# Kernel tuning notes

Measured on AMD Instinct MI355X. Metric: run time of the kernel, lower is better.

Reference implementation:

```python
import jax, jax.numpy as jnp
import numpy as np

N_IN = 2048
N_OUT = 2048
RANK = 64
NUM_ITER = 4  # Newton-Schulz iterations, matches default num_iter=4


def setup_inputs() -> dict:
    key = jax.random.key(0)
    k1, k2, k3 = jax.random.split(key, 3)
    # scale U,V modestly so A = UV^T - VU^T is well-conditioned (mimics orthogonal init scale)
    scale = 1.0 / np.sqrt(N_IN)
    return {
        "input": jax.random.normal(k1, (8, 2048, N_IN), dtype=jnp.float32),
        "U": jax.random.normal(k2, (N_IN, RANK), dtype=jnp.float32) * scale,
        "V": jax.random.normal(k3, (N_IN, RANK), dtype=jnp.float32) * scale,
    }


def _orthogonal_weight(U, V):
    # A = U V^T - V U^T  (skew-symmetric, rank <= 2*rank)
    A = U @ V.T - V @ U.T              # [n, n]
    I = jnp.eye(N_IN, dtype=A.dtype)
    B = I - A
    X = I
    for _ in range(NUM_ITER):          # Newton-Schulz iteration for B^{-1}
        X = X @ (2.0 * I - B @ X)
    W_square = (I + A) @ X             # Cayley transform (I+A)(I-A)^{-1} approx
    return W_square[:N_OUT, :N_IN]


def reference(input, U, V):
    W = _orthogonal_weight(U, V)       # [out, in]
    # F.linear(input, W) = input @ W.T
    return jnp.einsum("bsi,oi->bso", input, W)
```

## Files before the change

kernel.cpp:

```cpp
#include <hip/hip_runtime.h>
#include <hip/hip_bf16.h>
#include <cstdint>
#include <cstddef>

#define NIN   2048
#define RANK  64
#define R2    128
#define NROWS 16384

typedef __bf16 bf16x8 __attribute__((ext_vector_type(8)));
typedef float  f32x4  __attribute__((ext_vector_type(4)));
typedef unsigned short u16x8 __attribute__((ext_vector_type(8)));

__device__ __forceinline__ unsigned short f2bf(float f) {
  union { float f; unsigned u; } x; x.f = f;
  return (unsigned short)((x.u + 0x7fffu + ((x.u >> 16) & 1u)) >> 16);
}

__device__ __forceinline__ void smallGemm(const float* __restrict__ A,
                                          const float* __restrict__ B,
                                          float* __restrict__ O,
                                          float a, float b, int t, int tid) {
  int i = (t >> 3) * 16 + (tid >> 4);
  int j = (t & 7) * 16 + (tid & 15);
  float acc = 0.f;
#pragma unroll 8
  for (int k = 0; k < R2; ++k) {
    float av = A[i * R2 + k]; if (k == i) av += a;
    float bv = B[k * R2 + j]; if (k == j) bv += b;
    acc += av * bv;
  }
  O[i * R2 + j] = acc;
}

__global__ __launch_bounds__(512) void k_prep(const float* __restrict__ U,
                                              const float* __restrict__ V,
                                              unsigned short* __restrict__ Mf,
                                              float* __restrict__ G) {
  __shared__ float red[512];
  int b = blockIdx.x, tid = threadIdx.x;
  if (b < 64) {
    int CI = b * 512 + tid;
    int lane = CI & 63, J = (CI >> 6) & 63, t = CI >> 12;
    int n = t * 16 + (lane & 15);
    int k0 = J * 32 + (lane >> 4) * 8;
    const float* src = (n < RANK) ? (U + n) : (V + (n - RANK));
    u16x8 h;
#pragma unroll
    for (int e = 0; e < 8; ++e) h[e] = f2bf(src[(size_t)(k0 + e) * RANK]);
    *(u16x8*)(Mf + (size_t)CI * 8) = h;
  } else {
    int tile = b - 64;
    int bi = tile >> 3, bj = tile & 7;
    int sub = tid >> 8, t256 = tid & 255;
    int ty = t256 >> 4, tx = t256 & 15;
    int i = bi * 16 + ty, j = bj * 16 + tx;
    const float* Ai = (i < RANK) ? (U + i) : (V + (i - RANK));
    const float* Aj = (j < RANK) ? (U + j) : (V + (j - RANK));
    int k0 = sub * 1024;
    float acc = 0.f;
#pragma unroll 8
    for (int k = k0; k < k0 + 1024; ++k) acc += Ai[(size_t)k * RANK] * Aj[(size_t)k * RANK];
    red[tid] = acc;
    __syncthreads();
    if (sub == 0) {
      float s = red[t256] + red[256 + t256];
      if (i < RANK) G[(i + RANK) * R2 + j] = -s;
      else          G[(i - RANK) * R2 + j] =  s;
    }
  }
}

struct SOp { const float* A; const float* B; float* O; float a, b; };
struct SOps { SOp op[3]; };
__global__ void k_small(SOps ops) {
  SOp o = ops.op[blockIdx.x >> 6];
  smallGemm(o.A, o.B, o.O, o.a, o.b, blockIdx.x & 63, threadIdx.x);
}

__global__ void k_D(const float* __restrict__ U, const float* __restrict__ V,
                    const float* __restrict__ H, const float* __restrict__ G15,
                    unsigned short* __restrict__ Df) {
  int idx = blockIdx.x * 256 + threadIdx.x;
  int i = idx >> 7, j = idx & 127;
  int jj = (j < RANK) ? (j + RANK) : (j - RANK);
  float sgn = (j < RANK) ? -1.f : 1.f;
  float acc = 0.f;
#pragma unroll 8
  for (int k = 0; k < R2; ++k) {
    float m = (k < RANK) ? U[(size_t)i * RANK + k] : V[(size_t)i * RANK + (k - RANK)];
    float t = 2.f * H[k * R2 + jj] - G15[k * R2 + jj];
    acc += m * (sgn * t);
  }
  int t_ = i >> 4, lr = i & 15;
  int J = j >> 5, lg = (j >> 3) & 3, e = j & 7;
  size_t CI = (size_t)(t_ * 4 + J) * 64 + lg * 16 + lr;
  Df[CI * 8 + e] = f2bf(acc);
}

__global__ __launch_bounds__(256) void k_T1(const float* __restrict__ input,
                                            const unsigned short* __restrict__ Mf,
                                            unsigned short* __restrict__ T1bf,
                                            const float* __restrict__ G,
                                            float* __restrict__ G2) {
  __shared__ __align__(16) unsigned char lds[73728];
  if (blockIdx.x >= 512) {
    smallGemm(G, G, G2, 0.f, 0.f, blockIdx.x - 512, threadIdx.x);
    return;
  }
  const int tid = threadIdx.x, lane = tid & 63, w = tid >> 6;
  const int lr = lane & 15, lg = lane >> 4;
  const int row0 = blockIdx.x * 32;
  unsigned char* abuf = lds + w * 8192;
  float* rbuf = (float*)lds;

  f32x4 acc[2][8] = {};
  const float* gbase = input + (size_t)row0 * NIN + w * 512;
  const int Jbase = w * 16;
  float4 s0[8], s1[8];
  bf16x8 bx[8], by[8];

#define T1_SLOAD(KT)                                                          \
  _Pragma("unroll") for (int p = 0; p < 8; ++p) {                             \
    int id = p * 64 + lane; int r = id >> 4, C = id & 15;                     \
    const float* g = gbase + (size_t)r * NIN + (KT) * 128 + C * 8;            \
    s0[p] = *(const float4*)g; s1[p] = *(const float4*)(g + 4);               \
  }
#define T1_SWRITE()                                                           \
  _Pragma("unroll") for (int p = 0; p < 8; ++p) {                             \
    int id = p * 64 + lane; int r = id >> 4, C = id & 15;                     \
    u16x8 h;                                                                  \
    h[0] = f2bf(s0[p].x); h[1] = f2bf(s0[p].y);                               \
    h[2] = f2bf(s0[p].z); h[3] = f2bf(s0[p].w);                               \
    h[4] = f2bf(s1[p].x); h[5] = f2bf(s1[p].y);                               \
    h[6] = f2bf(s1[p].z); h[7] = f2bf(s1[p].w);                               \
    *(u16x8*)(abuf + r * 256 + ((C ^ (r & 7)) << 4)) = h;                     \
  }
#define T1_BLOAD(P, S)                                                        \
  _Pragma("unroll") for (int t = 0; t < 8; ++t)                               \
    P[t] = *(const bf16x8*)(Mf + ((size_t)(t * 64 + Jbase + (S)) * 64 + lane) * 8);

  T1_SLOAD(0);
  T1_SWRITE();
  T1_BLOAD(bx, 0);
#pragma unroll
  for (int s = 0; s < 16; ++s) {
    const int kt = s >> 2, j = s & 3;
    if (j == 0 && kt < 3) { T1_SLOAD(kt + 1); }
    bf16x8 a0, a1;
    {
      int C = j * 4 + lg;
      a0 = *(const bf16x8*)(abuf + lr * 256 + ((C ^ (lr & 7)) << 4));
      a1 = *(const bf16x8*)(abuf + (16 + lr) * 256 + ((C ^ ((16 + lr) & 7)) << 4));
    }
    if (s < 15) { if (s & 1) { T1_BLOAD(bx, s + 1); } else { T1_BLOAD(by, s + 1); } }
#pragma unroll
    for (int t = 0; t < 8; ++t) {
      bf16x8 bcur = (s & 1) ? by[t] : bx[t];
      acc[0][t] = __builtin_amdgcn_mfma_f32_16x16x32_bf16(a0, bcur, acc[0][t], 0, 0, 0);
      acc[1][t] = __builtin_amdgcn_mfma_f32_16x16x32_bf16(a1, bcur, acc[1][t], 0, 0, 0);
    }
    if (j == 3 && kt < 3) { T1_SWRITE(); }
  }

  __syncthreads();
#pragma unroll
  for (int m = 0; m < 2; ++m)
#pragma unroll
    for (int t = 0; t < 8; ++t) {
      int col = t * 16 + lr, row = m * 16 + lg * 4;
      *(f32x4*)&rbuf[((size_t)w * 128 + col) * 36 + row] = acc[m][t];
    }
  __syncthreads();
  {
    int r = tid & 31, cg = tid >> 5;
    u16x8 o1, o2;
#pragma unroll
    for (int i = 0; i < 16; ++i) {
      int col = cg * 16 + i;
      float s = rbuf[(size_t)col * 36 + r]
              + rbuf[((size_t)128 + col) * 36 + r]
              + rbuf[((size_t)256 + col) * 36 + r]
              + rbuf[((size_t)384 + col) * 36 + r];
      if (i < 8) o1[i] = f2bf(s); else o2[i - 8] = f2bf(s);
    }
    unsigned short* dst = T1bf + (size_t)(row0 + r) * R2 + cg * 16;
    *(u16x8*)dst = o1;
    *(u16x8*)(dst + 8) = o2;
  }
}

__global__ __launch_bounds__(256) void k_OUT(const float* __restrict__ input,
                                             const unsigned short* __restrict__ T1bf,
                                             const unsigned short* __restrict__ Df,
                                             float* __restrict__ out) {
  __shared__ float obuf[4][32][132];
  const int tid = threadIdx.x, lane = tid & 63, w = tid >> 6;
  const int lr = lane & 15, lg = lane >> 4;
  const int row0 = blockIdx.x * 32;

  bf16x8 bq[2][4];
#pragma unroll
  for (int R = 0; R < 2; ++R)
#pragma unroll
    for (int J = 0; J < 4; ++J)
      bq[R][J] = *(const bf16x8*)(T1bf + (size_t)(row0 + R * 16 + lr) * R2 + J * 32 + lg * 8);

  bf16x8 xd[4], yd[4];
#define O_DLOAD(P, TTI)                                                       \
  _Pragma("unroll") for (int J = 0; J < 4; ++J)                               \
    P[J] = *(const bf16x8*)(Df + ((size_t)((w * 32 + (TTI)) * 4 + J) * 64 + lane) * 8);

  O_DLOAD(xd, 0);
#pragma unroll
  for (int g = 0; g < 4; ++g) {
#pragma unroll
    for (int tt = 0; tt < 8; ++tt) {
      const int tti = g * 8 + tt;
      if (tti < 31) { if (tti & 1) { O_DLOAD(xd, tti + 1); } else { O_DLOAD(yd, tti + 1); } }
#pragma unroll
      for (int R = 0; R < 2; ++R) {
        f32x4 o = {};
#pragma unroll
        for (int J = 0; J < 4; ++J) {
          bf16x8 d = (tti & 1) ? yd[J] : xd[J];
          o = __builtin_amdgcn_mfma_f32_16x16x32_bf16(d, bq[R][J], o, 0, 0, 0);
        }
        *(f32x4*)&obuf[w][R * 16 + lr][tt * 16 + lg * 4] = o;
      }
    }
#pragma unroll
    for (int c = 0; c < 16; ++c) {
      int id = c * 64 + lane;
      int r = id >> 5, cc = id & 31;
      f32x4 v = *(const f32x4*)&obuf[w][r][cc * 4];
      int grow = row0 + r, gcol = w * 512 + g * 128 + cc * 4;
      float4 inv = *(const float4*)(input + (size_t)grow * NIN + gcol);
      float4 res = { v[0] + inv.x, v[1] + inv.y, v[2] + inv.z, v[3] + inv.w };
      *(float4*)(out + (size_t)grow * NIN + gcol) = res;
    }
  }
}

extern "C" void kernel_launch(void* const* d_in, const int* in_sizes, int n_in,
                              void* d_out, int out_size, void* d_ws, size_t ws_size,
                              hipStream_t stream) {
  const float* input = (const float*)d_in[0];
  const float* U     = (const float*)d_in[1];
  const float* V     = (const float*)d_in[2];
  float* out = (float*)d_out;
  char* ws = (char*)d_ws;

  float* mats = (float*)ws;
  float* G   = mats + 0 * 16384;
  float* G2  = mats + 1 * 16384;
  float* G3  = mats + 2 * 16384;
  float* G4  = mats + 3 * 16384;
  float* G7  = mats + 4 * 16384;
  float* G8  = mats + 5 * 16384;
  float* H12 = mats + 6 * 16384;
  float* H124= mats + 7 * 16384;
  float* H   = mats + 8 * 16384;
  float* G15 = mats + 9 * 16384;
  unsigned short* Mf   = (unsigned short*)(ws + 10 * 65536);
  unsigned short* Df   = (unsigned short*)(ws + 10 * 65536 + 524288);
  unsigned short* T1bf = (unsigned short*)(ws + 10 * 65536 + 2 * 524288);

  k_prep<<<128, 512, 0, stream>>>(U, V, Mf, G);
  k_T1<<<576, 256, 0, stream>>>(input, Mf, T1bf, G, G2);

  { SOps o = {{ {G2, G2, G4, 0.f, 0.f}, {G2, G, G3, 0.f, 0.f}, {G, G2, H12, 1.f, 1.f} }};
    k_small<<<192, 256, 0, stream>>>(o); }
  { SOps o = {{ {G4, G4, G8, 0.f, 0.f}, {G3, G4, G7, 0.f, 0.f}, {H12, G4, H124, 0.f, 1.f} }};
    k_small<<<192, 256, 0, stream>>>(o); }
  { SOps o = {{ {G7, G8, G15, 0.f, 0.f}, {H124, G8, H, 0.f, 1.f}, {nullptr,nullptr,nullptr,0.f,0.f} }};
    k_small<<<128, 256, 0, stream>>>(o); }

  k_D<<<1024, 256, 0, stream>>>(U, V, H, G15, Df);
  k_OUT<<<512, 256, 0, stream>>>(input, T1bf, Df, out);
}
```

Baseline: 159.5 us.

## Fold D-matrix kernel into output kernel via reassociated low-rank product

```diff
diff --git a/kernel.cpp b/kernel.cpp
--- a/kernel.cpp
+++ b/kernel.cpp
@@ -36,6 +36,7 @@
 __global__ __launch_bounds__(512) void k_prep(const float* __restrict__ U,
                                               const float* __restrict__ V,
                                               unsigned short* __restrict__ Mf,
+                                              unsigned short* __restrict__ Mrf,
                                               float* __restrict__ G) {
   __shared__ float red[512];
   int b = blockIdx.x, tid = threadIdx.x;
@@ -49,7 +50,7 @@
 #pragma unroll
     for (int e = 0; e < 8; ++e) h[e] = f2bf(src[(size_t)(k0 + e) * RANK]);
     *(u16x8*)(Mf + (size_t)CI * 8) = h;
-  } else {
+  } else if (b < 128) {
     int tile = b - 64;
     int bi = tile >> 3, bj = tile & 7;
     int sub = tid >> 8, t256 = tid & 255;
@@ -58,16 +59,34 @@
     const float* Ai = (i < RANK) ? (U + i) : (V + (i - RANK));
     const float* Aj = (j < RANK) ? (U + j) : (V + (j - RANK));
     int k0 = sub * 1024;
-    float acc = 0.f;
-#pragma unroll 8
-    for (int k = k0; k < k0 + 1024; ++k) acc += Ai[(size_t)k * RANK] * Aj[(size_t)k * RANK];
-    red[tid] = acc;
+    float p0 = 0.f, p1 = 0.f, p2 = 0.f, p3 = 0.f;
+#pragma unroll 4
+    for (int k = k0; k < k0 + 1024; k += 4) {
+      p0 += Ai[(size_t)k * RANK]       * Aj[(size_t)k * RANK];
+      p1 += Ai[(size_t)(k + 1) * RANK] * Aj[(size_t)(k + 1) * RANK];
+      p2 += Ai[(size_t)(k + 2) * RANK] * Aj[(size_t)(k + 2) * RANK];
+      p3 += Ai[(size_t)(k + 3) * RANK] * Aj[(size_t)(k + 3) * RANK];
+    }
+    red[tid] = (p0 + p1) + (p2 + p3);
     __syncthreads();
     if (sub == 0) {
       float s = red[t256] + red[256 + t256];
       if (i < RANK) G[(i + RANK) * R2 + j] = -s;
       else          G[(i - RANK) * R2 + j] =  s;
     }
+  } else {
+    int CI = (b - 128) * 512 + tid;
+    int lane = CI & 63, rest = CI >> 6;
+    int lr = lane & 15, lg = lane >> 4;
+    int J = rest & 3, t_ = rest >> 2;
+    int i = t_ * 16 + lr, j0 = J * 32 + lg * 8;
+    const float* src = (j0 < RANK) ? (U + (size_t)i * RANK + j0)
+                                   : (V + (size_t)i * RANK + (j0 - RANK));
+    float4 f0 = *(const float4*)src, f1 = *(const float4*)(src + 4);
+    u16x8 h;
+    h[0] = f2bf(f0.x); h[1] = f2bf(f0.y); h[2] = f2bf(f0.z); h[3] = f2bf(f0.w);
+    h[4] = f2bf(f1.x); h[5] = f2bf(f1.y); h[6] = f2bf(f1.z); h[7] = f2bf(f1.w);
+    *(u16x8*)(Mrf + (size_t)CI * 8) = h;
   }
 }
 
@@ -76,26 +95,6 @@
 __global__ void k_small(SOps ops) {
   SOp o = ops.op[blockIdx.x >> 6];
   smallGemm(o.A, o.B, o.O, o.a, o.b, blockIdx.x & 63, threadIdx.x);
-}
-
-__global__ void k_D(const float* __restrict__ U, const float* __restrict__ V,
-                    const float* __restrict__ H, const float* __restrict__ G15,
-                    unsigned short* __restrict__ Df) {
-  int idx = blockIdx.x * 256 + threadIdx.x;
-  int i = idx >> 7, j = idx & 127;
-  int jj = (j < RANK) ? (j + RANK) : (j - RANK);
-  float sgn = (j < RANK) ? -1.f : 1.f;
-  float acc = 0.f;
-#pragma unroll 8
-  for (int k = 0; k < R2; ++k) {
-    float m = (k < RANK) ? U[(size_t)i * RANK + k] : V[(size_t)i * RANK + (k - RANK)];
-    float t = 2.f * H[k * R2 + jj] - G15[k * R2 + jj];
-    acc += m * (sgn * t);
-  }
-  int t_ = i >> 4, lr = i & 15;
-  int J = j >> 5, lg = (j >> 3) & 3, e = j & 7;
-  size_t CI = (size_t)(t_ * 4 + J) * 64 + lg * 16 + lr;
-  Df[CI * 8 + e] = f2bf(acc);
 }
 
 __global__ __launch_bounds__(256) void k_T1(const float* __restrict__ input,
@@ -192,24 +191,84 @@
 
 __global__ __launch_bounds__(256) void k_OUT(const float* __restrict__ input,
                                              const unsigned short* __restrict__ T1bf,
-                                             const unsigned short* __restrict__ Df,
+                                             const float* __restrict__ Hm,
+                                             const float* __restrict__ G15m,
+                                             const unsigned short* __restrict__ Mrf,
                                              float* __restrict__ out) {
-  __shared__ float obuf[4][32][132];
+  __shared__ __align__(16) unsigned char lds[75776];
+  unsigned char* cbuf = lds;
+  unsigned char* t2buf = lds + 67584;
   const int tid = threadIdx.x, lane = tid & 63, w = tid >> 6;
   const int lr = lane & 15, lg = lane >> 4;
   const int row0 = blockIdx.x * 32;
 
+#pragma unroll
+  for (int it = 0; it < 8; ++it) {
+    int id = it * 256 + tid;
+    int k = id >> 4, j8 = id & 15, j0 = j8 * 8;
+    int jj0 = (j0 < RANK) ? j0 + RANK : j0 - RANK;
+    float sgn = (j0 < RANK) ? -1.f : 1.f;
+    const float* hp = Hm + k * R2 + jj0;
+    const float* gp = G15m + k * R2 + jj0;
+    float4 h0 = *(const float4*)hp, h1 = *(const float4*)(hp + 4);
+    float4 g0 = *(const float4*)gp, g1 = *(const float4*)(gp + 4);
+    u16x8 cv;
+    cv[0] = f2bf(sgn * (2.f * h0.x - g0.x));
+    cv[1] = f2bf(sgn * (2.f * h0.y - g0.y));
+    cv[2] = f2bf(sgn * (2.f * h0.z - g0.z));
+    cv[3] = f2bf(sgn * (2.f * h0.w - g0.w));
+    cv[4] = f2bf(sgn * (2.f * h1.x - g1.x));
+    cv[5] = f2bf(sgn * (2.f * h1.y - g1.y));
+    cv[6] = f2bf(sgn * (2.f * h1.z - g1.z));
+    cv[7] = f2bf(sgn * (2.f * h1.w - g1.w));
+    *(u16x8*)(cbuf + k * 256 + ((j8 ^ (k & 7)) << 4)) = cv;
+  }
+  bf16x8 t1f[2][4];
+#pragma unroll
+  for (int R = 0; R < 2; ++R)
+#pragma unroll
+    for (int J = 0; J < 4; ++J)
+      t1f[R][J] = *(const bf16x8*)(T1bf + (size_t)(row0 + R * 16 + lr) * R2 + J * 32 + lg * 8);
+  __syncthreads();
+
+#pragma unroll
+  for (int kk = 0; kk < 2; ++kk) {
+    int kct = w * 2 + kk;
+    int kc = kct * 16 + lr;
+    f32x4 a2[2] = {};
+#pragma unroll
+    for (int jkt = 0; jkt < 4; ++jkt) {
+      bf16x8 cf = *(const bf16x8*)(cbuf + kc * 256 + (((jkt * 4 + lg) ^ (kc & 7)) << 4));
+#pragma unroll
+      for (int R = 0; R < 2; ++R)
+        a2[R] = __builtin_amdgcn_mfma_f32_16x16x32_bf16(cf, t1f[R][jkt], a2[R], 0, 0, 0);
+    }
+#pragma unroll
+    for (int R = 0; R < 2; ++R) {
+      int r = R * 16 + lr;
+      ushort4 p;
+      p.x = f2bf(a2[R][0]); p.y = f2bf(a2[R][1]);
+      p.z = f2bf(a2[R][2]); p.w = f2bf(a2[R][3]);
+      int gran = kct * 2 + (lg >> 1), off = (lg & 1) * 8;
+      *(ushort4*)(t2buf + r * 256 + ((gran ^ (r & 7)) << 4) + off) = p;
+    }
+  }
+  __syncthreads();
+
   bf16x8 bq[2][4];
 #pragma unroll
   for (int R = 0; R < 2; ++R)
 #pragma unroll
-    for (int J = 0; J < 4; ++J)
-      bq[R][J] = *(const bf16x8*)(T1bf + (size_t)(row0 + R * 16 + lr) * R2 + J * 32 + lg * 8);
-
+    for (int J = 0; J < 4; ++J) {
+      int row = R * 16 + lr;
+      bq[R][J] = *(const bf16x8*)(t2buf + row * 256 + (((J * 4 + lg) ^ (row & 7)) << 4));
+    }
+
+  float* obufw = (float*)lds + (size_t)w * 32 * 132;
   bf16x8 xd[4], yd[4];
 #define O_DLOAD(P, TTI)                                                       \
   _Pragma("unroll") for (int J = 0; J < 4; ++J)                               \
-    P[J] = *(const bf16x8*)(Df + ((size_t)((w * 32 + (TTI)) * 4 + J) * 64 + lane) * 8);
+    P[J] = *(const bf16x8*)(Mrf + ((size_t)((w * 32 + (TTI)) * 4 + J) * 64 + lane) * 8);
 
   O_DLOAD(xd, 0);
 #pragma unroll
@@ -226,14 +285,14 @@
           bf16x8 d = (tti & 1) ? yd[J] : xd[J];
           o = __builtin_amdgcn_mfma_f32_16x16x32_bf16(d, bq[R][J], o, 0, 0, 0);
         }
-        *(f32x4*)&obuf[w][R * 16 + lr][tt * 16 + lg * 4] = o;
+        *(f32x4*)&obufw[(R * 16 + lr) * 132 + tt * 16 + lg * 4] = o;
       }
     }
 #pragma unroll
     for (int c = 0; c < 16; ++c) {
       int id = c * 64 + lane;
       int r = id >> 5, cc = id & 31;
-      f32x4 v = *(const f32x4*)&obuf[w][r][cc * 4];
+      f32x4 v = *(const f32x4*)&obufw[r * 132 + cc * 4];
       int grow = row0 + r, gcol = w * 512 + g * 128 + cc * 4;
       float4 inv = *(const float4*)(input + (size_t)grow * NIN + gcol);
       float4 res = { v[0] + inv.x, v[1] + inv.y, v[2] + inv.z, v[3] + inv.w };
@@ -263,10 +322,10 @@
   float* H   = mats + 8 * 16384;
   float* G15 = mats + 9 * 16384;
   unsigned short* Mf   = (unsigned short*)(ws + 10 * 65536);
-  unsigned short* Df   = (unsigned short*)(ws + 10 * 65536 + 524288);
+  unsigned short* Mrf  = (unsigned short*)(ws + 10 * 65536 + 524288);
   unsigned short* T1bf = (unsigned short*)(ws + 10 * 65536 + 2 * 524288);
 
-  k_prep<<<128, 512, 0, stream>>>(U, V, Mf, G);
+  k_prep<<<192, 512, 0, stream>>>(U, V, Mf, Mrf, G);
   k_T1<<<576, 256, 0, stream>>>(input, Mf, T1bf, G, G2);
 
   { SOps o = {{ {G2, G2, G4, 0.f, 0.f}, {G2, G, G3, 0.f, 0.f}, {G, G2, H12, 1.f, 1.f} }};
@@ -276,6 +335,5 @@
   { SOps o = {{ {G7, G8, G15, 0.f, 0.f}, {H124, G8, H, 0.f, 1.f}, {nullptr,nullptr,nullptr,0.f,0.f} }};
     k_small<<<128, 256, 0, stream>>>(o); }
 
-  k_D<<<1024, 256, 0, stream>>>(U, V, H, G15, Df);
-  k_OUT<<<512, 256, 0, stream>>>(input, T1bf, Df, out);
-}
+  k_OUT<<<512, 256, 0, stream>>>(input, T1bf, H, G15, Mrf, out);
+}
```

After: 141.3 us. 11.4% less time.
